# Kernel optimization log

Hardware: AMD Instinct MI355X
Metric: run time of the kernel (lower is better)

Reference implementation:

```python
import jax, jax.numpy as jnp
import numpy as np

T, B, I, H, LBL = 200, 1024, 128, 128, 4


def setup_inputs() -> dict:
    key = jax.random.key(0)
    ks = jax.random.split(key, 14)
    si = 1.0 / np.sqrt(I)
    sh = 1.0 / np.sqrt(H)
    inputs = jax.random.normal(ks[0], (T, B, I), jnp.float32)
    lengths = jnp.maximum(jax.random.randint(ks[1], (B,), 1, T + 1), LBL).astype(jnp.int32)
    return {
        "inputs": inputs,
        "lengths": lengths,
        "Wih_g": jax.random.normal(ks[2], (3 * H, I), jnp.float32) * si,
        "Whh_g": jax.random.normal(ks[3], (3 * H, H), jnp.float32) * sh,
        "bih_g": jax.random.normal(ks[4], (3 * H,), jnp.float32) * sh,
        "bhh_g": jax.random.normal(ks[5], (3 * H,), jnp.float32) * sh,
        "Wih_l": jax.random.normal(ks[6], (3 * H, I), jnp.float32) * si,
        "Whh_l": jax.random.normal(ks[7], (3 * H, H), jnp.float32) * sh,
        "bih_l": jax.random.normal(ks[8], (3 * H,), jnp.float32) * sh,
        "bhh_l": jax.random.normal(ks[9], (3 * H,), jnp.float32) * sh,
        "A1": jax.random.normal(ks[10], (H, H), jnp.float32) * sh,
        "A2": jax.random.normal(ks[11], (H, H), jnp.float32) * sh,
        "v1": jax.random.normal(ks[12], (1, H), jnp.float32) * sh,
        "label_len": LBL,
    }


def gru(x, Wih, Whh, bih, bhh):
    # x: [T, B, I] time-major. PyTorch GRU cell semantics.
    Bq, Hq = x.shape[1], Whh.shape[1]
    gi_all = jnp.einsum('tbi,gi->tbg', x, Wih) + bih  # precompute input projections [T,B,3H]
    def step(h, gi):
        gh = h @ Whh.T + bhh
        ir, iz, inn = jnp.split(gi, 3, axis=-1)
        hr, hz, hn = jnp.split(gh, 3, axis=-1)
        r = jax.nn.sigmoid(ir + hr)
        z = jax.nn.sigmoid(iz + hz)
        n = jnp.tanh(inn + r * hn)
        h = (1.0 - z) * n + z * h
        return h, h
    h0 = jnp.zeros((Bq, Hq), x.dtype)
    _, hs = jax.lax.scan(step, h0, gi_all)
    return hs  # [T, B, H]


def reference(inputs, lengths, Wih_g, Whh_g, bih_g, bhh_g,
              Wih_l, Whh_l, bih_l, bhh_l, A1, A2, v1, label_len):
    h_g = gru(inputs, Wih_g, Whh_g, bih_g, bhh_g)  # [T,B,H]
    h_l = gru(inputs, Wih_l, Whh_l, bih_l, bhh_l)  # [T,B,H]
    # attention score per step s: v1(sigmoid(A1 h_l + A2 h_g)), query-independent
    pre = jax.nn.sigmoid(jnp.einsum('tbh,gh->tbg', h_l, A1) +
                         jnp.einsum('tbh,gh->tbg', h_g, A2))
    scores = jnp.einsum('tbg,og->tbo', pre, v1)  # [T,B,1]
    # per-t output = cumsum_{s<=t}(score*h_l) + h_g[t]
    out = jnp.cumsum(scores * h_l, axis=0) + h_g  # [T,B,H]
    out_b = jnp.transpose(out, (1, 0, 2))  # [B,T,H]
    # gather last label_len timesteps of each sequence: h[b,k] = out[L_b-label_len+k, b]
    idx = lengths[:, None].astype(jnp.int32) - label_len + jnp.arange(label_len, dtype=jnp.int32)[None, :]
    idx = jnp.clip(idx, 0, out_b.shape[1] - 1)  # [B, label_len]
    h = jnp.take_along_axis(out_b, idx[:, :, None], axis=1)  # [B, label_len, H]
    return h
```

## Files before the change

### kernel.cpp

```cpp
#include <hip/hip_runtime.h>
#include <stdint.h>


typedef __attribute__((ext_vector_type(8))) short short8;
typedef __attribute__((ext_vector_type(4))) float float4v;

#define LDS_BARRIER() asm volatile("s_waitcnt lgkmcnt(0)\n\ts_barrier" ::: "memory")

__device__ inline float bf2f(unsigned short u){
  union { unsigned int i; float f; } v; v.i = ((unsigned int)u) << 16; return v.f;
}
__device__ inline unsigned short f2bf(float f){
  union { float f; unsigned int i; } v; v.f = f;
  unsigned int x = v.i;
  return (unsigned short)((x + 0x7fffu + ((x >> 16) & 1u)) >> 16);
}
__device__ inline unsigned int cvt_pk_bf16(float a, float b){
  unsigned int r;
  asm("v_cvt_pk_bf16_f32 %0, %1, %2" : "=v"(r) : "v"(a), "v"(b));
  return r;
}
__device__ inline float sigm(float x){ return __builtin_amdgcn_rcpf(1.0f + __expf(-x)); }

union __align__(16) LdsU {
  struct { unsigned short hbuf[2][16][136]; unsigned short xbuf[2][16][136]; } scan;
  struct {
    unsigned short hlL[25 * 544];
    unsigned short hgL[25 * 544];
    float part[8 * 112];
    float scR[112];
  } cm;
};

__global__ __launch_bounds__(512, 2) void k_fat(
    const float* __restrict__ x,
    const float* __restrict__ bih_g, const float* __restrict__ bhh_g,
    const float* __restrict__ bih_l, const float* __restrict__ bhh_l,
    const float* __restrict__ Wih_g, const float* __restrict__ Whh_g,
    const float* __restrict__ Wih_l, const float* __restrict__ Whh_l,
    unsigned short* __restrict__ wst, unsigned short* __restrict__ a12,
    const float* __restrict__ v1, const int* __restrict__ lengths,
    unsigned short* __restrict__ hl, unsigned short* __restrict__ hg,
    float* __restrict__ cum, float* __restrict__ out,
    int scan_t0, int sccum_t0, int sccum_base, int build)
{
  __shared__ LdsU lds;
  int tid = threadIdx.x;
  int bid = blockIdx.x;

  if (scan_t0 >= 0 && bid < 128) {
    const int tc = 100;
    int t0 = scan_t0;
    auto& hbuf = lds.scan.hbuf;
    auto& xbuf = lds.scan.xbuf;

    int w = tid >> 6, L = tid & 63, l15 = L & 15, q = L >> 4;
    int gru = bid & 1;
    int b0 = (bid >> 1) * 16;
    const float* bih = gru ? bih_l : bih_g;
    const float* bhh = gru ? bhh_l : bhh_g;
    unsigned short* myseq = gru ? hl : hg;

    int col = w * 16 + l15;

    short8 Wi[3][4], Wh[3][4];
    if (t0 == 0) {
      const float* Wih = gru ? Wih_l : Wih_g;
      const float* Whh = gru ? Whh_l : Whh_g;
      #pragma unroll
      for (int G = 0; G < 3; G++) {
        int row = G * 128 + col;
        #pragma unroll
        for (int kf = 0; kf < 4; kf++) {
          const float4* p0 = (const float4*)(Wih + (size_t)row * 128 + kf * 32 + q * 8);
          const float4* p1 = (const float4*)(Whh + (size_t)row * 128 + kf * 32 + q * 8);
          float4 a0 = p0[0], a1 = p0[1], b0f = p1[0], b1f = p1[1];
          short8 si, sh;
          si[0]=(short)f2bf(a0.x); si[1]=(short)f2bf(a0.y); si[2]=(short)f2bf(a0.z); si[3]=(short)f2bf(a0.w);
          si[4]=(short)f2bf(a1.x); si[5]=(short)f2bf(a1.y); si[6]=(short)f2bf(a1.z); si[7]=(short)f2bf(a1.w);
          sh[0]=(short)f2bf(b0f.x); sh[1]=(short)f2bf(b0f.y); sh[2]=(short)f2bf(b0f.z); sh[3]=(short)f2bf(b0f.w);
          sh[4]=(short)f2bf(b1f.x); sh[5]=(short)f2bf(b1f.y); sh[6]=(short)f2bf(b1f.z); sh[7]=(short)f2bf(b1f.w);
          Wi[G][kf] = si; Wh[G][kf] = sh;
        }
      }
    } else {
      int gmi = gru * 2;
      int gmh = gru * 2 + 1;
      #pragma unroll
      for (int G = 0; G < 3; G++) {
        #pragma unroll
        for (int kf = 0; kf < 4; kf++) {
          Wi[G][kf] = *(const short8*)(wst + (((size_t)((gmi * 3 + G) * 4 + kf)) << 12) + tid * 8);
          Wh[G][kf] = *(const short8*)(wst + (((size_t)((gmh * 3 + G) * 4 + kf)) << 12) + tid * 8);
        }
      }
    }
    float br  = bih[col]       + bhh[col];
    float bz  = bih[128 + col] + bhh[128 + col];
    float bin = bih[256 + col];
    float bnh = bhh[256 + col];

    float hold[4];
    if (t0 == 0) {
      #pragma unroll
      for (int r = 0; r < 4; r++) { hold[r] = 0.0f; hbuf[0][q * 4 + r][col] = 0; }
    } else {
      const unsigned short* carry = myseq + (size_t)(t0 - 1) * 131072;
      #pragma unroll
      for (int r = 0; r < 4; r++) {
        int m = q * 4 + r;
        unsigned short u = carry[(size_t)(b0 + m) * 128 + col];
        hold[r] = bf2f(u);
        hbuf[0][m][col] = u;
      }
    }
    int xrow = tid >> 5, xc4 = (tid & 31) * 4;
    size_t hoff = (size_t)b0 * 128 + xrow * 128 + xc4;
    {
      float4 x0 = ((const float4*)(x + ((size_t)t0 * 1024 + b0) * 128))[tid];
      *(uint2*)&xbuf[0][xrow][xc4] = make_uint2(cvt_pk_bf16(x0.x, x0.y), cvt_pk_bf16(x0.z, x0.w));
    }
    float4 xr = ((const float4*)(x + ((size_t)(t0 + 1) * 1024 + b0) * 128))[tid];
    __syncthreads();

    float4v cx0 = (float4v){0.f,0.f,0.f,0.f}, cx1 = cx0, cx2 = cx0;
    {
      short8 Ax[4];
      #pragma unroll
      for (int kf = 0; kf < 4; kf++) Ax[kf] = *(const short8*)&xbuf[0][l15][kf * 32 + q * 8];
      #pragma unroll
      for (int kf = 0; kf < 4; kf++) cx0 = __builtin_amdgcn_mfma_f32_16x16x32_bf16(Ax[kf], Wi[0][kf], cx0, 0,0,0);
      #pragma unroll
      for (int kf = 0; kf < 4; kf++) cx1 = __builtin_amdgcn_mfma_f32_16x16x32_bf16(Ax[kf], Wi[1][kf], cx1, 0,0,0);
      #pragma unroll
      for (int kf = 0; kf < 4; kf++) cx2 = __builtin_amdgcn_mfma_f32_16x16x32_bf16(Ax[kf], Wi[2][kf], cx2, 0,0,0);
    }
    *(uint2*)&xbuf[1][xrow][xc4] = make_uint2(cvt_pk_bf16(xr.x, xr.y), cvt_pk_bf16(xr.z, xr.w));
    xr = ((const float4*)(x + ((size_t)(t0 + 2) * 1024 + b0) * 128))[tid];
    LDS_BARRIER();

    auto step = [&](int s, int pin, int pout) {
      short8 Ah[4], Axn[4];
      #pragma unroll
      for (int kf = 0; kf < 4; kf++) Ah[kf]  = *(const short8*)&hbuf[pin][l15][kf * 32 + q * 8];
      #pragma unroll
      for (int kf = 0; kf < 4; kf++) Axn[kf] = *(const short8*)&xbuf[pout][l15][kf * 32 + q * 8];

      if (s > 0) {
        uint2 hv = *(const uint2*)&hbuf[pin][xrow][xc4];
        *(uint2*)(myseq + (size_t)(t0 + s - 1) * 131072 + hoff) = hv;
      }

      float4v rh = (float4v){0.f,0.f,0.f,0.f}, zh = rh, nh = rh;
      #pragma unroll
      for (int kf = 0; kf < 4; kf++) rh = __builtin_amdgcn_mfma_f32_16x16x32_bf16(Ah[kf], Wh[0][kf], rh, 0,0,0);
      #pragma unroll
      for (int kf = 0; kf < 4; kf++) zh = __builtin_amdgcn_mfma_f32_16x16x32_bf16(Ah[kf], Wh[1][kf], zh, 0,0,0);
      #pragma unroll
      for (int kf = 0; kf < 4; kf++) nh = __builtin_amdgcn_mfma_f32_16x16x32_bf16(Ah[kf], Wh[2][kf], nh, 0,0,0);

      float4v nx0 = (float4v){0.f,0.f,0.f,0.f}, nx1 = nx0, nx2 = nx0;
      #pragma unroll
      for (int kf = 0; kf < 4; kf++) nx0 = __builtin_amdgcn_mfma_f32_16x16x32_bf16(Axn[kf], Wi[0][kf], nx0, 0,0,0);
      #pragma unroll
      for (int kf = 0; kf < 4; kf++) nx1 = __builtin_amdgcn_mfma_f32_16x16x32_bf16(Axn[kf], Wi[1][kf], nx1, 0,0,0);
      #pragma unroll
      for (int kf = 0; kf < 4; kf++) nx2 = __builtin_amdgcn_mfma_f32_16x16x32_bf16(Axn[kf], Wi[2][kf], nx2, 0,0,0);

      *(uint2*)&xbuf[pin][xrow][xc4] = make_uint2(cvt_pk_bf16(xr.x, xr.y), cvt_pk_bf16(xr.z, xr.w));
      {
        int t3 = t0 + (s + 3 < tc ? s + 3 : tc - 1);
        xr = ((const float4*)(x + ((size_t)t3 * 1024 + b0) * 128))[tid];
      }

      float cr[4], cz[4], cn[4];
      #pragma unroll
      for (int r = 0; r < 4; r++) { cr[r] = cx0[r] + br; cz[r] = cx1[r] + bz; cn[r] = cx2[r] + bin; }

      float hnv[4];
      #pragma unroll
      for (int r = 0; r < 4; r++) {
        float er = __expf(-(rh[r] + cr[r]));
        float ez = __expf(-(zh[r] + cz[r]));
        float pr = 1.0f + er, pz = 1.0f + ez;
        float inv = __builtin_amdgcn_rcpf(pr * pz);
        float rr = pz * inv;
        float zz = pr * inv;
        float y  = cn[r] + rr * (nh[r] + bnh);
        float em = __expf(-2.0f * y);
        float nn = 2.0f * __builtin_amdgcn_rcpf(1.0f + em) - 1.0f;
        hnv[r] = nn + zz * (hold[r] - nn);
        hold[r] = hnv[r];
      }
      unsigned int p01 = cvt_pk_bf16(hnv[0], hnv[1]);
      unsigned int p23 = cvt_pk_bf16(hnv[2], hnv[3]);
      hbuf[pout][q * 4 + 0][col] = (unsigned short)p01;
      hbuf[pout][q * 4 + 1][col] = (unsigned short)(p01 >> 16);
      hbuf[pout][q * 4 + 2][col] = (unsigned short)p23;
      hbuf[pout][q * 4 + 3][col] = (unsigned short)(p23 >> 16);

      cx0 = nx0; cx1 = nx1; cx2 = nx2;
      LDS_BARRIER();
    };

    for (int s = 0; s + 1 < tc; s += 2) { step(s, 0, 1); step(s + 1, 1, 0); }
    {
      uint2 hv = *(const uint2*)&hbuf[tc & 1][xrow][xc4];
      *(uint2*)(myseq + (size_t)(t0 + tc - 1) * 131072 + hoff) = hv;
    }
    return;
  }

  if (build) {
    if (bid < 128) return;
    int gid = (bid - 128) * 512 + tid;
    (void)gid;
    return;
  }

  if (sccum_t0 >= 0) {
    int t0c = sccum_t0;
    int rb = bid - sccum_base;
    int b0c = rb * 4;
    int w = tid >> 6, L = tid & 63, l15 = L & 15, q = L >> 4;
    int jc = tid & 127, bc = tid >> 7;
    int b = b0c + bc;

    auto* hlL = lds.cm.hlL;
    auto* hgL = lds.cm.hgL;
    float* part = lds.cm.part;
    float* scR  = lds.cm.scR;

    float c = (t0c == 0) ? 0.0f : cum[(size_t)b * 128 + jc];
    int cap0 = lengths[b] - 4;

    float hgv[4];
    #pragma unroll
    for (int d = 0; d < 4; d++) {
      int sl = cap0 + d - t0c;
      hgv[d] = (sl >= 0 && sl < 100) ? bf2f(hg[((size_t)(cap0 + d) * 1024 + b) * 128 + jc]) : 0.f;
    }

    short8 B1[4], B2[4];
    #pragma unroll
    for (int kf = 0; kf < 4; kf++) {
      B1[kf] = *(const short8*)(a12 + (size_t)(w * 16 + l15) * 128 + kf * 32 + q * 8);
      B2[kf] = *(const short8*)(a12 + 16384 + (size_t)(w * 16 + l15) * 128 + kf * 32 + q * 8);
    }
    float v1w = v1[w * 16 + l15];

    for (int seg = 0; seg < 4; seg++) {
      int t0s = t0c + seg * 25;
      __syncthreads();
      for (int f8 = tid; f8 < 1600; f8 += 512) {
        int sl = f8 >> 6, r8 = f8 & 63, bb = r8 >> 4, j8 = r8 & 15;
        size_t gsrc = ((size_t)(t0s + sl) * 1024 + b0c) * 128 + r8 * 8;
        int dst = sl * 544 + bb * 136 + j8 * 8;
        *(short8*)&hlL[dst] = *(const short8*)(hl + gsrc);
        *(short8*)&hgL[dst] = *(const short8*)(hg + gsrc);
      }
      __syncthreads();

      #pragma unroll
      for (int T = 0; T < 7; T++) {
        int tl = T * 4 + (l15 >> 2); if (tl > 24) tl = 24;
        int bb = l15 & 3;
        int abase = tl * 544 + bb * 136 + q * 8;
        short8 Al[4], Ag[4];
        #pragma unroll
        for (int kf = 0; kf < 4; kf++) {
          Al[kf] = *(const short8*)&hlL[abase + kf * 32];
          Ag[kf] = *(const short8*)&hgL[abase + kf * 32];
        }
        float4v acc = (float4v){0.f, 0.f, 0.f, 0.f};
        #pragma unroll
        for (int kf = 0; kf < 4; kf++) acc = __builtin_amdgcn_mfma_f32_16x16x32_bf16(Al[kf], B1[kf], acc, 0,0,0);
        #pragma unroll
        for (int kf = 0; kf < 4; kf++) acc = __builtin_amdgcn_mfma_f32_16x16x32_bf16(Ag[kf], B2[kf], acc, 0,0,0);
        #pragma unroll
        for (int r = 0; r < 4; r++) {
          float sv = v1w * sigm(acc[r]);
          sv += __shfl_xor(sv, 1, 16);
          sv += __shfl_xor(sv, 2, 16);
          sv += __shfl_xor(sv, 4, 16);
          sv += __shfl_xor(sv, 8, 16);
          if (l15 == 0) part[w * 112 + T * 16 + q * 4 + r] = sv;
        }
      }
      __syncthreads();
      if (tid < 100) {
        float s = 0.f;
        #pragma unroll
        for (int w8 = 0; w8 < 8; w8++) s += part[w8 * 112 + tid];
        scR[tid] = s;
      }
      __syncthreads();

      for (int sl = 0; sl < 25; sl += 5) {
        float h[5], scv[5];
        #pragma unroll
        for (int k = 0; k < 5; k++) {
          h[k]  = bf2f(hlL[(sl + k) * 544 + bc * 136 + jc]);
          scv[k] = scR[(sl + k) * 4 + bc];
        }
        #pragma unroll
        for (int k = 0; k < 5; k++) {
          c += scv[k] * h[k];
          int d = (t0s + sl + k) - cap0;
          if ((unsigned)d < 4u)
            out[((size_t)b * 4 + d) * 128 + jc] = c + hgv[d];
        }
      }
    }
    cum[(size_t)b * 128 + jc] = c;
    return;
  }
}

__global__ __launch_bounds__(512) void k_build(
    const float* __restrict__ Wih_g, const float* __restrict__ Whh_g,
    const float* __restrict__ Wih_l, const float* __restrict__ Whh_l,
    const float* __restrict__ A1, const float* __restrict__ A2,
    unsigned short* __restrict__ wst, unsigned short* __restrict__ a12)
{
  int gid = blockIdx.x * 512 + threadIdx.x;
  if (gid < 32768) a12[gid] = f2bf((gid < 16384) ? A1[gid] : A2[gid - 16384]);
  #pragma unroll
  for (int k = 0; k < 3; k++) {
    int i = gid + k * 65536;
    int f = i >> 12;
    int r = i & 4095;
    int t = r >> 3, e = r & 7;
    int l15 = t & 15, q = (t >> 4) & 3, wv = t >> 6;
    int col = wv * 16 + l15;
    int kf = f & 3, g3 = f >> 2;
    int G = g3 % 3, gm = g3 / 3;
    const float* src = (gm == 0) ? Wih_g : (gm == 1) ? Whh_g : (gm == 2) ? Wih_l : Whh_l;
    int row = G * 128 + col;
    int kk = kf * 32 + q * 8 + e;
    wst[i] = f2bf(src[(size_t)row * 128 + kk]);
  }
}

extern "C" void kernel_launch(void* const* d_in, const int* in_sizes, int n_in,
                              void* d_out, int out_size, void* d_ws, size_t ws_size,
                              hipStream_t stream)
{
  const float* x     = (const float*)d_in[0];
  const int* lengths = (const int*)d_in[1];
  const float* Wih_g = (const float*)d_in[2];
  const float* Whh_g = (const float*)d_in[3];
  const float* bih_g = (const float*)d_in[4];
  const float* bhh_g = (const float*)d_in[5];
  const float* Wih_l = (const float*)d_in[6];
  const float* Whh_l = (const float*)d_in[7];
  const float* bih_l = (const float*)d_in[8];
  const float* bhh_l = (const float*)d_in[9];
  const float* A1    = (const float*)d_in[10];
  const float* A2    = (const float*)d_in[11];
  const float* v1    = (const float*)d_in[12];
  float* out = (float*)d_out;

  char* wsb = (char*)d_ws;
  size_t o = 0;
  unsigned short* a12 = (unsigned short*)(wsb + o); o += 65536;
  unsigned short* wst = (unsigned short*)(wsb + o); o += 393216;
  float* cum          = (float*)(wsb + o);          o += 524288;
  unsigned short* hl  = (unsigned short*)(wsb + o); o += (size_t)200 * 1024 * 128 * 2;
  unsigned short* hg  = (unsigned short*)(wsb + o); o += (size_t)200 * 1024 * 128 * 2;
  if (o > ws_size) return;

  k_build<<<128, 512, 0, stream>>>(Wih_g, Whh_g, Wih_l, Whh_l, A1, A2, wst, a12);
  k_fat<<<128, 512, 0, stream>>>(x, bih_g, bhh_g, bih_l, bhh_l,
                                 Wih_g, Whh_g, Wih_l, Whh_l,
                                 wst, a12, v1, lengths, hl, hg, cum, out,
                                 0, -1, 0, 0);
  k_fat<<<384, 512, 0, stream>>>(x, bih_g, bhh_g, bih_l, bhh_l,
                                 Wih_g, Whh_g, Wih_l, Whh_l,
                                 wst, a12, v1, lengths, hl, hg, cum, out,
                                 100, 0, 128, 0);
  k_fat<<<256, 512, 0, stream>>>(x, bih_g, bhh_g, bih_l, bhh_l,
                                 Wih_g, Whh_g, Wih_l, Whh_l,
                                 wst, a12, v1, lengths, hl, hg, cum, out,
                                 -1, 100, 0, 0);
}
```

Measured before the change: 398.6 us.

## Pack two independent scan groups per 1024-thread block with LDS spin barriers

Each 1024-thread block now holds two independent 16-batch GRU scan halves, which synchronise through per-half LDS atomic counters and spin-waits instead of a block-wide s_barrier. The idea is that one half's gate math and MFMAs can overlap the other half's barrier wait on the same CU. Grids are halved to match, the cum/score phase runs two instances per block, and the first scan now always loads prebuilt bf16 weights. Risks are spin-wait overhead, fewer CUs used (64 blocks for the scan) and possible livelock if waves are not co-resident.

```diff
diff --git a/kernel.cpp b/kernel.cpp
--- a/kernel.cpp
+++ b/kernel.cpp
@@ -4,8 +4,6 @@
 
 typedef __attribute__((ext_vector_type(8))) short short8;
 typedef __attribute__((ext_vector_type(4))) float float4v;
-
-#define LDS_BARRIER() asm volatile("s_waitcnt lgkmcnt(0)\n\ts_barrier" ::: "memory")
 
 __device__ inline float bf2f(unsigned short u){
   union { unsigned int i; float f; } v; v.i = ((unsigned int)u) << 16; return v.f;
@@ -21,301 +19,6 @@
   return r;
 }
 __device__ inline float sigm(float x){ return __builtin_amdgcn_rcpf(1.0f + __expf(-x)); }
-
-union __align__(16) LdsU {
-  struct { unsigned short hbuf[2][16][136]; unsigned short xbuf[2][16][136]; } scan;
-  struct {
-    unsigned short hlL[25 * 544];
-    unsigned short hgL[25 * 544];
-    float part[8 * 112];
-    float scR[112];
-  } cm;
-};
-
-__global__ __launch_bounds__(512, 2) void k_fat(
-    const float* __restrict__ x,
-    const float* __restrict__ bih_g, const float* __restrict__ bhh_g,
-    const float* __restrict__ bih_l, const float* __restrict__ bhh_l,
-    const float* __restrict__ Wih_g, const float* __restrict__ Whh_g,
-    const float* __restrict__ Wih_l, const float* __restrict__ Whh_l,
-    unsigned short* __restrict__ wst, unsigned short* __restrict__ a12,
-    const float* __restrict__ v1, const int* __restrict__ lengths,
-    unsigned short* __restrict__ hl, unsigned short* __restrict__ hg,
-    float* __restrict__ cum, float* __restrict__ out,
-    int scan_t0, int sccum_t0, int sccum_base, int build)
-{
-  __shared__ LdsU lds;
-  int tid = threadIdx.x;
-  int bid = blockIdx.x;
-
-  if (scan_t0 >= 0 && bid < 128) {
-    const int tc = 100;
-    int t0 = scan_t0;
-    auto& hbuf = lds.scan.hbuf;
-    auto& xbuf = lds.scan.xbuf;
-
-    int w = tid >> 6, L = tid & 63, l15 = L & 15, q = L >> 4;
-    int gru = bid & 1;
-    int b0 = (bid >> 1) * 16;
-    const float* bih = gru ? bih_l : bih_g;
-    const float* bhh = gru ? bhh_l : bhh_g;
-    unsigned short* myseq = gru ? hl : hg;
-
-    int col = w * 16 + l15;
-
-    short8 Wi[3][4], Wh[3][4];
-    if (t0 == 0) {
-      const float* Wih = gru ? Wih_l : Wih_g;
-      const float* Whh = gru ? Whh_l : Whh_g;
-      #pragma unroll
-      for (int G = 0; G < 3; G++) {
-        int row = G * 128 + col;
-        #pragma unroll
-        for (int kf = 0; kf < 4; kf++) {
-          const float4* p0 = (const float4*)(Wih + (size_t)row * 128 + kf * 32 + q * 8);
-          const float4* p1 = (const float4*)(Whh + (size_t)row * 128 + kf * 32 + q * 8);
-          float4 a0 = p0[0], a1 = p0[1], b0f = p1[0], b1f = p1[1];
-          short8 si, sh;
-          si[0]=(short)f2bf(a0.x); si[1]=(short)f2bf(a0.y); si[2]=(short)f2bf(a0.z); si[3]=(short)f2bf(a0.w);
-          si[4]=(short)f2bf(a1.x); si[5]=(short)f2bf(a1.y); si[6]=(short)f2bf(a1.z); si[7]=(short)f2bf(a1.w);
-          sh[0]=(short)f2bf(b0f.x); sh[1]=(short)f2bf(b0f.y); sh[2]=(short)f2bf(b0f.z); sh[3]=(short)f2bf(b0f.w);
-          sh[4]=(short)f2bf(b1f.x); sh[5]=(short)f2bf(b1f.y); sh[6]=(short)f2bf(b1f.z); sh[7]=(short)f2bf(b1f.w);
-          Wi[G][kf] = si; Wh[G][kf] = sh;
-        }
-      }
-    } else {
-      int gmi = gru * 2;
-      int gmh = gru * 2 + 1;
-      #pragma unroll
-      for (int G = 0; G < 3; G++) {
-        #pragma unroll
-        for (int kf = 0; kf < 4; kf++) {
-          Wi[G][kf] = *(const short8*)(wst + (((size_t)((gmi * 3 + G) * 4 + kf)) << 12) + tid * 8);
-          Wh[G][kf] = *(const short8*)(wst + (((size_t)((gmh * 3 + G) * 4 + kf)) << 12) + tid * 8);
-        }
-      }
-    }
-    float br  = bih[col]       + bhh[col];
-    float bz  = bih[128 + col] + bhh[128 + col];
-    float bin = bih[256 + col];
-    float bnh = bhh[256 + col];
-
-    float hold[4];
-    if (t0 == 0) {
-      #pragma unroll
-      for (int r = 0; r < 4; r++) { hold[r] = 0.0f; hbuf[0][q * 4 + r][col] = 0; }
-    } else {
-      const unsigned short* carry = myseq + (size_t)(t0 - 1) * 131072;
-      #pragma unroll
-      for (int r = 0; r < 4; r++) {
-        int m = q * 4 + r;
-        unsigned short u = carry[(size_t)(b0 + m) * 128 + col];
-        hold[r] = bf2f(u);
-        hbuf[0][m][col] = u;
-      }
-    }
-    int xrow = tid >> 5, xc4 = (tid & 31) * 4;
-    size_t hoff = (size_t)b0 * 128 + xrow * 128 + xc4;
-    {
-      float4 x0 = ((const float4*)(x + ((size_t)t0 * 1024 + b0) * 128))[tid];
-      *(uint2*)&xbuf[0][xrow][xc4] = make_uint2(cvt_pk_bf16(x0.x, x0.y), cvt_pk_bf16(x0.z, x0.w));
-    }
-    float4 xr = ((const float4*)(x + ((size_t)(t0 + 1) * 1024 + b0) * 128))[tid];
-    __syncthreads();
-
-    float4v cx0 = (float4v){0.f,0.f,0.f,0.f}, cx1 = cx0, cx2 = cx0;
-    {
-      short8 Ax[4];
-      #pragma unroll
-      for (int kf = 0; kf < 4; kf++) Ax[kf] = *(const short8*)&xbuf[0][l15][kf * 32 + q * 8];
-      #pragma unroll
-      for (int kf = 0; kf < 4; kf++) cx0 = __builtin_amdgcn_mfma_f32_16x16x32_bf16(Ax[kf], Wi[0][kf], cx0, 0,0,0);
-      #pragma unroll
-      for (int kf = 0; kf < 4; kf++) cx1 = __builtin_amdgcn_mfma_f32_16x16x32_bf16(Ax[kf], Wi[1][kf], cx1, 0,0,0);
-      #pragma unroll
-      for (int kf = 0; kf < 4; kf++) cx2 = __builtin_amdgcn_mfma_f32_16x16x32_bf16(Ax[kf], Wi[2][kf], cx2, 0,0,0);
-    }
-    *(uint2*)&xbuf[1][xrow][xc4] = make_uint2(cvt_pk_bf16(xr.x, xr.y), cvt_pk_bf16(xr.z, xr.w));
-    xr = ((const float4*)(x + ((size_t)(t0 + 2) * 1024 + b0) * 128))[tid];
-    LDS_BARRIER();
-
-    auto step = [&](int s, int pin, int pout) {
-      short8 Ah[4], Axn[4];
-      #pragma unroll
-      for (int kf = 0; kf < 4; kf++) Ah[kf]  = *(const short8*)&hbuf[pin][l15][kf * 32 + q * 8];
-      #pragma unroll
-      for (int kf = 0; kf < 4; kf++) Axn[kf] = *(const short8*)&xbuf[pout][l15][kf * 32 + q * 8];
-
-      if (s > 0) {
-        uint2 hv = *(const uint2*)&hbuf[pin][xrow][xc4];
-        *(uint2*)(myseq + (size_t)(t0 + s - 1) * 131072 + hoff) = hv;
-      }
-
-      float4v rh = (float4v){0.f,0.f,0.f,0.f}, zh = rh, nh = rh;
-      #pragma unroll
-      for (int kf = 0; kf < 4; kf++) rh = __builtin_amdgcn_mfma_f32_16x16x32_bf16(Ah[kf], Wh[0][kf], rh, 0,0,0);
-      #pragma unroll
-      for (int kf = 0; kf < 4; kf++) zh = __builtin_amdgcn_mfma_f32_16x16x32_bf16(Ah[kf], Wh[1][kf], zh, 0,0,0);
-      #pragma unroll
-      for (int kf = 0; kf < 4; kf++) nh = __builtin_amdgcn_mfma_f32_16x16x32_bf16(Ah[kf], Wh[2][kf], nh, 0,0,0);
-
-      float4v nx0 = (float4v){0.f,0.f,0.f,0.f}, nx1 = nx0, nx2 = nx0;
-      #pragma unroll
-      for (int kf = 0; kf < 4; kf++) nx0 = __builtin_amdgcn_mfma_f32_16x16x32_bf16(Axn[kf], Wi[0][kf], nx0, 0,0,0);
-      #pragma unroll
-      for (int kf = 0; kf < 4; kf++) nx1 = __builtin_amdgcn_mfma_f32_16x16x32_bf16(Axn[kf], Wi[1][kf], nx1, 0,0,0);
-      #pragma unroll
-      for (int kf = 0; kf < 4; kf++) nx2 = __builtin_amdgcn_mfma_f32_16x16x32_bf16(Axn[kf], Wi[2][kf], nx2, 0,0,0);
-
-      *(uint2*)&xbuf[pin][xrow][xc4] = make_uint2(cvt_pk_bf16(xr.x, xr.y), cvt_pk_bf16(xr.z, xr.w));
-      {
-        int t3 = t0 + (s + 3 < tc ? s + 3 : tc - 1);
-        xr = ((const float4*)(x + ((size_t)t3 * 1024 + b0) * 128))[tid];
-      }
-
-      float cr[4], cz[4], cn[4];
-      #pragma unroll
-      for (int r = 0; r < 4; r++) { cr[r] = cx0[r] + br; cz[r] = cx1[r] + bz; cn[r] = cx2[r] + bin; }
-
-      float hnv[4];
-      #pragma unroll
-      for (int r = 0; r < 4; r++) {
-        float er = __expf(-(rh[r] + cr[r]));
-        float ez = __expf(-(zh[r] + cz[r]));
-        float pr = 1.0f + er, pz = 1.0f + ez;
-        float inv = __builtin_amdgcn_rcpf(pr * pz);
-        float rr = pz * inv;
-        float zz = pr * inv;
-        float y  = cn[r] + rr * (nh[r] + bnh);
-        float em = __expf(-2.0f * y);
-        float nn = 2.0f * __builtin_amdgcn_rcpf(1.0f + em) - 1.0f;
-        hnv[r] = nn + zz * (hold[r] - nn);
-        hold[r] = hnv[r];
-      }
-      unsigned int p01 = cvt_pk_bf16(hnv[0], hnv[1]);
-      unsigned int p23 = cvt_pk_bf16(hnv[2], hnv[3]);
-      hbuf[pout][q * 4 + 0][col] = (unsigned short)p01;
-      hbuf[pout][q * 4 + 1][col] = (unsigned short)(p01 >> 16);
-      hbuf[pout][q * 4 + 2][col] = (unsigned short)p23;
-      hbuf[pout][q * 4 + 3][col] = (unsigned short)(p23 >> 16);
-
-      cx0 = nx0; cx1 = nx1; cx2 = nx2;
-      LDS_BARRIER();
-    };
-
-    for (int s = 0; s + 1 < tc; s += 2) { step(s, 0, 1); step(s + 1, 1, 0); }
-    {
-      uint2 hv = *(const uint2*)&hbuf[tc & 1][xrow][xc4];
-      *(uint2*)(myseq + (size_t)(t0 + tc - 1) * 131072 + hoff) = hv;
-    }
-    return;
-  }
-
-  if (build) {
-    if (bid < 128) return;
-    int gid = (bid - 128) * 512 + tid;
-    (void)gid;
-    return;
-  }
-
-  if (sccum_t0 >= 0) {
-    int t0c = sccum_t0;
-    int rb = bid - sccum_base;
-    int b0c = rb * 4;
-    int w = tid >> 6, L = tid & 63, l15 = L & 15, q = L >> 4;
-    int jc = tid & 127, bc = tid >> 7;
-    int b = b0c + bc;
-
-    auto* hlL = lds.cm.hlL;
-    auto* hgL = lds.cm.hgL;
-    float* part = lds.cm.part;
-    float* scR  = lds.cm.scR;
-
-    float c = (t0c == 0) ? 0.0f : cum[(size_t)b * 128 + jc];
-    int cap0 = lengths[b] - 4;
-
-    float hgv[4];
-    #pragma unroll
-    for (int d = 0; d < 4; d++) {
-      int sl = cap0 + d - t0c;
-      hgv[d] = (sl >= 0 && sl < 100) ? bf2f(hg[((size_t)(cap0 + d) * 1024 + b) * 128 + jc]) : 0.f;
-    }
-
-    short8 B1[4], B2[4];
-    #pragma unroll
-    for (int kf = 0; kf < 4; kf++) {
-      B1[kf] = *(const short8*)(a12 + (size_t)(w * 16 + l15) * 128 + kf * 32 + q * 8);
-      B2[kf] = *(const short8*)(a12 + 16384 + (size_t)(w * 16 + l15) * 128 + kf * 32 + q * 8);
-    }
-    float v1w = v1[w * 16 + l15];
-
-    for (int seg = 0; seg < 4; seg++) {
-      int t0s = t0c + seg * 25;
-      __syncthreads();
-      for (int f8 = tid; f8 < 1600; f8 += 512) {
-        int sl = f8 >> 6, r8 = f8 & 63, bb = r8 >> 4, j8 = r8 & 15;
-        size_t gsrc = ((size_t)(t0s + sl) * 1024 + b0c) * 128 + r8 * 8;
-        int dst = sl * 544 + bb * 136 + j8 * 8;
-        *(short8*)&hlL[dst] = *(const short8*)(hl + gsrc);
-        *(short8*)&hgL[dst] = *(const short8*)(hg + gsrc);
-      }
-      __syncthreads();
-
-      #pragma unroll
-      for (int T = 0; T < 7; T++) {
-        int tl = T * 4 + (l15 >> 2); if (tl > 24) tl = 24;
-        int bb = l15 & 3;
-        int abase = tl * 544 + bb * 136 + q * 8;
-        short8 Al[4], Ag[4];
-        #pragma unroll
-        for (int kf = 0; kf < 4; kf++) {
-          Al[kf] = *(const short8*)&hlL[abase + kf * 32];
-          Ag[kf] = *(const short8*)&hgL[abase + kf * 32];
-        }
-        float4v acc = (float4v){0.f, 0.f, 0.f, 0.f};
-        #pragma unroll
-        for (int kf = 0; kf < 4; kf++) acc = __builtin_amdgcn_mfma_f32_16x16x32_bf16(Al[kf], B1[kf], acc, 0,0,0);
-        #pragma unroll
-        for (int kf = 0; kf < 4; kf++) acc = __builtin_amdgcn_mfma_f32_16x16x32_bf16(Ag[kf], B2[kf], acc, 0,0,0);
-        #pragma unroll
-        for (int r = 0; r < 4; r++) {
-          float sv = v1w * sigm(acc[r]);
-          sv += __shfl_xor(sv, 1, 16);
-          sv += __shfl_xor(sv, 2, 16);
-          sv += __shfl_xor(sv, 4, 16);
-          sv += __shfl_xor(sv, 8, 16);
-          if (l15 == 0) part[w * 112 + T * 16 + q * 4 + r] = sv;
-        }
-      }
-      __syncthreads();
-      if (tid < 100) {
-        float s = 0.f;
-        #pragma unroll
-        for (int w8 = 0; w8 < 8; w8++) s += part[w8 * 112 + tid];
-        scR[tid] = s;
-      }
-      __syncthreads();
-
-      for (int sl = 0; sl < 25; sl += 5) {
-        float h[5], scv[5];
-        #pragma unroll
-        for (int k = 0; k < 5; k++) {
-          h[k]  = bf2f(hlL[(sl + k) * 544 + bc * 136 + jc]);
-          scv[k] = scR[(sl + k) * 4 + bc];
-        }
-        #pragma unroll
-        for (int k = 0; k < 5; k++) {
-          c += scv[k] * h[k];
-          int d = (t0s + sl + k) - cap0;
-          if ((unsigned)d < 4u)
-            out[((size_t)b * 4 + d) * 128 + jc] = c + hgv[d];
-        }
-      }
-    }
-    cum[(size_t)b * 128 + jc] = c;
-    return;
-  }
-}
 
 __global__ __launch_bounds__(512) void k_build(
     const float* __restrict__ Wih_g, const float* __restrict__ Whh_g,
@@ -342,6 +45,290 @@
   }
 }
 
+union __align__(16) LdsU {
+  struct {
+    unsigned short hbuf[2][2][16][136];
+    unsigned short xbuf[2][2][16][136];
+    unsigned bar[2];
+  } scan;
+  struct CmI {
+    unsigned short hlL[25 * 544];
+    unsigned short hgL[25 * 544];
+    float part[8 * 112];
+    float scR[112];
+  } cm[2];
+};
+
+__global__ __launch_bounds__(1024, 1) void k_fat(
+    const float* __restrict__ x,
+    const float* __restrict__ bih_g, const float* __restrict__ bhh_g,
+    const float* __restrict__ bih_l, const float* __restrict__ bhh_l,
+    const unsigned short* __restrict__ wst, const unsigned short* __restrict__ a12,
+    const float* __restrict__ v1, const int* __restrict__ lengths,
+    unsigned short* __restrict__ hl, unsigned short* __restrict__ hg,
+    float* __restrict__ cum, float* __restrict__ out,
+    int scan_t0, int sccum_t0, int sccum_base)
+{
+  __shared__ LdsU lds;
+  int tid = threadIdx.x;
+  int bid = blockIdx.x;
+
+  if (scan_t0 >= 0 && bid < 64) {
+    const int tc = 100;
+    int t0 = scan_t0;
+    int t = tid & 511, half = tid >> 9;
+    unsigned short (&hbuf)[2][16][136] = lds.scan.hbuf[half];
+    unsigned short (&xbuf)[2][16][136] = lds.scan.xbuf[half];
+    volatile unsigned* bp = &lds.scan.bar[half];
+
+    int w = t >> 6, L = t & 63, l15 = L & 15, q = L >> 4;
+    int gru = bid & 1;
+    int b0 = ((bid >> 1) * 2 + half) * 16;
+    const float* bih = gru ? bih_l : bih_g;
+    const float* bhh = gru ? bhh_l : bhh_g;
+    unsigned short* myseq = gru ? hl : hg;
+
+    int col = w * 16 + l15;
+
+    short8 Wi[3][4], Wh[3][4];
+    {
+      int gmi = gru * 2, gmh = gru * 2 + 1;
+      #pragma unroll
+      for (int G = 0; G < 3; G++) {
+        #pragma unroll
+        for (int kf = 0; kf < 4; kf++) {
+          Wi[G][kf] = *(const short8*)(wst + (((size_t)((gmi * 3 + G) * 4 + kf)) << 12) + t * 8);
+          Wh[G][kf] = *(const short8*)(wst + (((size_t)((gmh * 3 + G) * 4 + kf)) << 12) + t * 8);
+        }
+      }
+    }
+    float br  = bih[col]       + bhh[col];
+    float bz  = bih[128 + col] + bhh[128 + col];
+    float bin = bih[256 + col];
+    float bnh = bhh[256 + col];
+
+    float hold[4];
+    if (t0 == 0) {
+      #pragma unroll
+      for (int r = 0; r < 4; r++) { hold[r] = 0.0f; hbuf[0][q * 4 + r][col] = 0; }
+    } else {
+      const unsigned short* carry = myseq + (size_t)(t0 - 1) * 131072;
+      #pragma unroll
+      for (int r = 0; r < 4; r++) {
+        int m = q * 4 + r;
+        unsigned short u = carry[(size_t)(b0 + m) * 128 + col];
+        hold[r] = bf2f(u);
+        hbuf[0][m][col] = u;
+      }
+    }
+    int xrow = t >> 5, xc4 = (t & 31) * 4;
+    size_t hoff = (size_t)b0 * 128 + xrow * 128 + xc4;
+    {
+      float4 x0 = ((const float4*)(x + ((size_t)t0 * 1024 + b0) * 128))[t];
+      *(uint2*)&xbuf[0][xrow][xc4] = make_uint2(cvt_pk_bf16(x0.x, x0.y), cvt_pk_bf16(x0.z, x0.w));
+    }
+    float4 xr = ((const float4*)(x + ((size_t)(t0 + 1) * 1024 + b0) * 128))[t];
+
+    if (tid < 2) lds.scan.bar[tid] = 0;
+    __syncthreads();
+
+    if (half) __builtin_amdgcn_s_sleep(15);
+
+    unsigned barcnt = 0;
+    auto half_bar = [&]() {
+      barcnt += 8;
+      asm volatile("s_waitcnt lgkmcnt(0)" ::: "memory");
+      if (L == 0) atomicAdd((unsigned*)&lds.scan.bar[half], 1u);
+      while (*bp < barcnt) { }
+      __builtin_amdgcn_sched_barrier(0);
+      asm volatile("" ::: "memory");
+    };
+
+    float4v cx0 = (float4v){0.f,0.f,0.f,0.f}, cx1 = cx0, cx2 = cx0;
+    {
+      short8 Ax[4];
+      #pragma unroll
+      for (int kf = 0; kf < 4; kf++) Ax[kf] = *(const short8*)&xbuf[0][l15][kf * 32 + q * 8];
+      #pragma unroll
+      for (int kf = 0; kf < 4; kf++) cx0 = __builtin_amdgcn_mfma_f32_16x16x32_bf16(Ax[kf], Wi[0][kf], cx0, 0,0,0);
+      #pragma unroll
+      for (int kf = 0; kf < 4; kf++) cx1 = __builtin_amdgcn_mfma_f32_16x16x32_bf16(Ax[kf], Wi[1][kf], cx1, 0,0,0);
+      #pragma unroll
+      for (int kf = 0; kf < 4; kf++) cx2 = __builtin_amdgcn_mfma_f32_16x16x32_bf16(Ax[kf], Wi[2][kf], cx2, 0,0,0);
+    }
+    *(uint2*)&xbuf[1][xrow][xc4] = make_uint2(cvt_pk_bf16(xr.x, xr.y), cvt_pk_bf16(xr.z, xr.w));
+    xr = ((const float4*)(x + ((size_t)(t0 + 2) * 1024 + b0) * 128))[t];
+    half_bar();
+
+    auto step = [&](int s, int pin, int pout) {
+      short8 Ah[4], Axn[4];
+      #pragma unroll
+      for (int kf = 0; kf < 4; kf++) Ah[kf]  = *(const short8*)&hbuf[pin][l15][kf * 32 + q * 8];
+      #pragma unroll
+      for (int kf = 0; kf < 4; kf++) Axn[kf] = *(const short8*)&xbuf[pout][l15][kf * 32 + q * 8];
+
+      if (s > 0) {
+        uint2 hv = *(const uint2*)&hbuf[pin][xrow][xc4];
+        *(uint2*)(myseq + (size_t)(t0 + s - 1) * 131072 + hoff) = hv;
+      }
+
+      float4v rh = (float4v){0.f,0.f,0.f,0.f}, zh = rh, nh = rh;
+      #pragma unroll
+      for (int kf = 0; kf < 4; kf++) rh = __builtin_amdgcn_mfma_f32_16x16x32_bf16(Ah[kf], Wh[0][kf], rh, 0,0,0);
+      #pragma unroll
+      for (int kf = 0; kf < 4; kf++) zh = __builtin_amdgcn_mfma_f32_16x16x32_bf16(Ah[kf], Wh[1][kf], zh, 0,0,0);
+      #pragma unroll
+      for (int kf = 0; kf < 4; kf++) nh = __builtin_amdgcn_mfma_f32_16x16x32_bf16(Ah[kf], Wh[2][kf], nh, 0,0,0);
+
+      float4v nx0 = (float4v){0.f,0.f,0.f,0.f}, nx1 = nx0, nx2 = nx0;
+      #pragma unroll
+      for (int kf = 0; kf < 4; kf++) nx0 = __builtin_amdgcn_mfma_f32_16x16x32_bf16(Axn[kf], Wi[0][kf], nx0, 0,0,0);
+      #pragma unroll
+      for (int kf = 0; kf < 4; kf++) nx1 = __builtin_amdgcn_mfma_f32_16x16x32_bf16(Axn[kf], Wi[1][kf], nx1, 0,0,0);
+      #pragma unroll
+      for (int kf = 0; kf < 4; kf++) nx2 = __builtin_amdgcn_mfma_f32_16x16x32_bf16(Axn[kf], Wi[2][kf], nx2, 0,0,0);
+
+      *(uint2*)&xbuf[pin][xrow][xc4] = make_uint2(cvt_pk_bf16(xr.x, xr.y), cvt_pk_bf16(xr.z, xr.w));
+      {
+        int t3 = t0 + (s + 3 < tc ? s + 3 : tc - 1);
+        xr = ((const float4*)(x + ((size_t)t3 * 1024 + b0) * 128))[t];
+      }
+
+      float cr[4], cz[4], cn[4];
+      #pragma unroll
+      for (int r = 0; r < 4; r++) { cr[r] = cx0[r] + br; cz[r] = cx1[r] + bz; cn[r] = cx2[r] + bin; }
+
+      float hnv[4];
+      #pragma unroll
+      for (int r = 0; r < 4; r++) {
+        float er = __expf(-(rh[r] + cr[r]));
+        float ez = __expf(-(zh[r] + cz[r]));
+        float pr = 1.0f + er, pz = 1.0f + ez;
+        float inv = __builtin_amdgcn_rcpf(pr * pz);
+        float rr = pz * inv;
+        float zz = pr * inv;
+        float y  = cn[r] + rr * (nh[r] + bnh);
+        float em = __expf(-2.0f * y);
+        float nn = 2.0f * __builtin_amdgcn_rcpf(1.0f + em) - 1.0f;
+        hnv[r] = nn + zz * (hold[r] - nn);
+        hold[r] = hnv[r];
+      }
+      unsigned int p01 = cvt_pk_bf16(hnv[0], hnv[1]);
+      unsigned int p23 = cvt_pk_bf16(hnv[2], hnv[3]);
+      hbuf[pout][q * 4 + 0][col] = (unsigned short)p01;
+      hbuf[pout][q * 4 + 1][col] = (unsigned short)(p01 >> 16);
+      hbuf[pout][q * 4 + 2][col] = (unsigned short)p23;
+      hbuf[pout][q * 4 + 3][col] = (unsigned short)(p23 >> 16);
+
+      cx0 = nx0; cx1 = nx1; cx2 = nx2;
+      half_bar();
+    };
+
+    for (int s = 0; s + 1 < tc; s += 2) { step(s, 0, 1); step(s + 1, 1, 0); }
+    {
+      uint2 hv = *(const uint2*)&hbuf[tc & 1][xrow][xc4];
+      *(uint2*)(myseq + (size_t)(t0 + tc - 1) * 131072 + hoff) = hv;
+    }
+    return;
+  }
+
+  if (sccum_t0 >= 0) {
+    int rb = bid - sccum_base;
+    if (rb < 0 || rb >= 128) return;
+    int inst = tid >> 9, t = tid & 511;
+    int t0c = sccum_t0;
+    int b0c = rb * 8 + inst * 4;
+    int w = t >> 6, L = t & 63, l15 = L & 15, q = L >> 4;
+    int jc = t & 127, bc = (t >> 7) & 3;
+    int b = b0c + bc;
+    auto& cmi = lds.cm[inst];
+
+    float c = (t0c == 0) ? 0.0f : cum[(size_t)b * 128 + jc];
+    int cap0 = lengths[b] - 4;
+
+    float hgv[4];
+    #pragma unroll
+    for (int d = 0; d < 4; d++) {
+      int sl = cap0 + d - t0c;
+      hgv[d] = (sl >= 0 && sl < 100) ? bf2f(hg[((size_t)(cap0 + d) * 1024 + b) * 128 + jc]) : 0.f;
+    }
+
+    short8 B1[4], B2[4];
+    #pragma unroll
+    for (int kf = 0; kf < 4; kf++) {
+      B1[kf] = *(const short8*)(a12 + (size_t)(w * 16 + l15) * 128 + kf * 32 + q * 8);
+      B2[kf] = *(const short8*)(a12 + 16384 + (size_t)(w * 16 + l15) * 128 + kf * 32 + q * 8);
+    }
+    float v1w = v1[w * 16 + l15];
+
+    for (int seg = 0; seg < 4; seg++) {
+      int t0s = t0c + seg * 25;
+      __syncthreads();
+      for (int f8 = t; f8 < 1600; f8 += 512) {
+        int sl = f8 >> 6, r8 = f8 & 63, bb = r8 >> 4, j8 = r8 & 15;
+        size_t gsrc = ((size_t)(t0s + sl) * 1024 + b0c) * 128 + r8 * 8;
+        int dst = sl * 544 + bb * 136 + j8 * 8;
+        *(short8*)&cmi.hlL[dst] = *(const short8*)(hl + gsrc);
+        *(short8*)&cmi.hgL[dst] = *(const short8*)(hg + gsrc);
+      }
+      __syncthreads();
+
+      #pragma unroll
+      for (int T = 0; T < 7; T++) {
+        int tl = T * 4 + (l15 >> 2); if (tl > 24) tl = 24;
+        int bb = l15 & 3;
+        int abase = tl * 544 + bb * 136 + q * 8;
+        short8 Al[4], Ag[4];
+        #pragma unroll
+        for (int kf = 0; kf < 4; kf++) {
+          Al[kf] = *(const short8*)&cmi.hlL[abase + kf * 32];
+          Ag[kf] = *(const short8*)&cmi.hgL[abase + kf * 32];
+        }
+        float4v acc = (float4v){0.f, 0.f, 0.f, 0.f};
+        #pragma unroll
+        for (int kf = 0; kf < 4; kf++) acc = __builtin_amdgcn_mfma_f32_16x16x32_bf16(Al[kf], B1[kf], acc, 0,0,0);
+        #pragma unroll
+        for (int kf = 0; kf < 4; kf++) acc = __builtin_amdgcn_mfma_f32_16x16x32_bf16(Ag[kf], B2[kf], acc, 0,0,0);
+        #pragma unroll
+        for (int r = 0; r < 4; r++) {
+          float sv = v1w * sigm(acc[r]);
+          sv += __shfl_xor(sv, 1, 16);
+          sv += __shfl_xor(sv, 2, 16);
+          sv += __shfl_xor(sv, 4, 16);
+          sv += __shfl_xor(sv, 8, 16);
+          if (l15 == 0) cmi.part[w * 112 + T * 16 + q * 4 + r] = sv;
+        }
+      }
+      __syncthreads();
+      if (t < 100) {
+        float s = 0.f;
+        #pragma unroll
+        for (int w8 = 0; w8 < 8; w8++) s += cmi.part[w8 * 112 + t];
+        cmi.scR[t] = s;
+      }
+      __syncthreads();
+
+      for (int sl = 0; sl < 25; sl += 5) {
+        float h[5], scv[5];
+        #pragma unroll
+        for (int k = 0; k < 5; k++) {
+          h[k]   = bf2f(cmi.hlL[(sl + k) * 544 + bc * 136 + jc]);
+          scv[k] = cmi.scR[(sl + k) * 4 + bc];
+        }
+        #pragma unroll
+        for (int k = 0; k < 5; k++) {
+          c += scv[k] * h[k];
+          int d = (t0s + sl + k) - cap0;
+          if ((unsigned)d < 4u)
+            out[((size_t)b * 4 + d) * 128 + jc] = c + hgv[d];
+        }
+      }
+    }
+    cum[(size_t)b * 128 + jc] = c;
+    return;
+  }
+}
+
 extern "C" void kernel_launch(void* const* d_in, const int* in_sizes, int n_in,
                               void* d_out, int out_size, void* d_ws, size_t ws_size,
                               hipStream_t stream)
@@ -371,16 +358,10 @@
   if (o > ws_size) return;
 
   k_build<<<128, 512, 0, stream>>>(Wih_g, Whh_g, Wih_l, Whh_l, A1, A2, wst, a12);
-  k_fat<<<128, 512, 0, stream>>>(x, bih_g, bhh_g, bih_l, bhh_l,
-                                 Wih_g, Whh_g, Wih_l, Whh_l,
-                                 wst, a12, v1, lengths, hl, hg, cum, out,
-                                 0, -1, 0, 0);
-  k_fat<<<384, 512, 0, stream>>>(x, bih_g, bhh_g, bih_l, bhh_l,
-                                 Wih_g, Whh_g, Wih_l, Whh_l,
-                                 wst, a12, v1, lengths, hl, hg, cum, out,
-                                 100, 0, 128, 0);
-  k_fat<<<256, 512, 0, stream>>>(x, bih_g, bhh_g, bih_l, bhh_l,
-                                 Wih_g, Whh_g, Wih_l, Whh_l,
-                                 wst, a12, v1, lengths, hl, hg, cum, out,
-                                 -1, 100, 0, 0);
-}
+  k_fat<<<64, 1024, 0, stream>>>(x, bih_g, bhh_g, bih_l, bhh_l, wst, a12, v1, lengths,
+                                 hl, hg, cum, out, 0, -1, 0);
+  k_fat<<<192, 1024, 0, stream>>>(x, bih_g, bhh_g, bih_l, bhh_l, wst, a12, v1, lengths,
+                                  hl, hg, cum, out, 100, 0, 64);
+  k_fat<<<128, 1024, 0, stream>>>(x, bih_g, bhh_g, bih_l, bhh_l, wst, a12, v1, lengths,
+                                  hl, hg, cum, out, -1, 100, 0);
+}
```

Result: slower. 1.469 ms (+268.6%).
